# Kernel optimization log

Measured on AMD Instinct MI355X. Metric: run time of the kernel, lower is better.

The kernel has to match this reference:

```python
import jax, jax.numpy as jnp
import numpy as np

B, L, D = 1, 4096, 2048
H, KV, HD = 16, 4, 128
WINDOW = 1024
ROPE_BASE = 10000.0


def _rms_norm(x, scale):
    var = jnp.mean(jnp.square(x), axis=-1, keepdims=True)
    return x * jax.lax.rsqrt(var + 1e-6) * scale


def _apply_rope(x, positions, base_frequency):
    # x: (B, L, N, HD); positions: (B, L)
    head_dim = x.shape[-1]
    half = head_dim // 2
    freq_exp = 2.0 * jnp.arange(half, dtype=jnp.float32) / head_dim
    timescale = base_frequency ** freq_exp                       # (half,)
    sinusoid = positions[..., None].astype(jnp.float32) / timescale  # (B, L, half)
    sin = jnp.sin(sinusoid)[:, :, None, :]                       # (B, L, 1, half)
    cos = jnp.cos(sinusoid)[:, :, None, :]
    x1, x2 = x[..., :half], x[..., half:]
    return jnp.concatenate([x1 * cos - x2 * sin, x2 * cos + x1 * sin], axis=-1)


def setup_inputs() -> dict:
    key = jax.random.key(0)
    ks = jax.random.split(key, 5)
    x = jax.random.normal(ks[0], (B, L, D), dtype=jnp.float32)
    positions = jnp.broadcast_to(jnp.arange(L, dtype=jnp.int32), (B, L))
    s = D ** -0.5
    Wq = jax.random.normal(ks[1], (D, H * HD), dtype=jnp.float32) * s
    Wk = jax.random.normal(ks[2], (D, KV * HD), dtype=jnp.float32) * s
    Wv = jax.random.normal(ks[3], (D, KV * HD), dtype=jnp.float32) * s
    Wo = jax.random.normal(ks[4], (H * HD, D), dtype=jnp.float32) * ((H * HD) ** -0.5)
    q_scale = jnp.ones((HD,), dtype=jnp.float32)
    k_scale = jnp.ones((HD,), dtype=jnp.float32)
    return {"x": x, "positions": positions, "Wq": Wq, "Wk": Wk, "Wv": Wv,
            "Wo": Wo, "q_scale": q_scale, "k_scale": k_scale}


def reference(x, positions, Wq, Wk, Wv, Wo, q_scale, k_scale):
    q = (x @ Wq).reshape(B, L, H, HD)
    k = (x @ Wk).reshape(B, L, KV, HD)
    v = (x @ Wv).reshape(B, L, KV, HD)

    q = _apply_rope(_rms_norm(q, q_scale), positions, ROPE_BASE)
    k = _apply_rope(_rms_norm(k, k_scale), positions, ROPE_BASE)

    rep = H // KV
    k = jnp.repeat(k, rep, axis=2)   # (B, L, H, HD)
    v = jnp.repeat(v, rep, axis=2)

    scale = HD ** -0.5
    scores = jnp.einsum('bqhd,bkhd->bhqk', q, k) * scale  # (B, H, L, L)

    idx = jnp.arange(L)
    causal = idx[:, None] >= idx[None, :]
    window = idx[None, :] >= idx[:, None] - (WINDOW - 1)
    mask = causal & window
    scores = jnp.where(mask[None, None, :, :], scores, jnp.finfo(scores.dtype).min)
    attn = jax.nn.softmax(scores, axis=-1)

    out = jnp.einsum('bhqk,bkhd->bqhd', attn, v).reshape(B, L, H * HD)
    return out @ Wo
```

## Files before the change

kernel.cpp:

```cpp
#include <hip/hip_runtime.h>
#include <cstdint>
#include <cstddef>

typedef unsigned short u16;
typedef __attribute__((ext_vector_type(4))) float  float4v;
typedef __attribute__((ext_vector_type(4))) int    int4v;
typedef __attribute__((ext_vector_type(8))) short  short8v;
typedef __attribute__((ext_vector_type(4))) short  short4v;

#define L_SEQ 4096
#define NH 16
#define NKV 4
#define WND 1024

static __device__ __forceinline__ u16 f2bf(float f) {
  union { float f; unsigned u; } v; v.f = f;
  unsigned r = (v.u + 0x7FFFu + ((v.u >> 16) & 1u)) >> 16;
  return (u16)r;
}
static __device__ __forceinline__ float bf2f(u16 b) {
  union { unsigned u; float f; } v; v.u = ((unsigned)b) << 16;
  return v.f;
}

__global__ __launch_bounds__(256) void k_cvt(const float* __restrict__ in,
                                             u16* __restrict__ out, int n4) {
  int i = blockIdx.x * 256 + threadIdx.x;
  if (i >= n4) return;
  float4v v = ((const float4v*)in)[i];
  short4v o;
  o[0] = (short)f2bf(v[0]); o[1] = (short)f2bf(v[1]);
  o[2] = (short)f2bf(v[2]); o[3] = (short)f2bf(v[3]);
  ((short4v*)out)[i] = o;
}

__global__ __launch_bounds__(256) void k_transpose64(const float* __restrict__ in,
                                                     u16* __restrict__ out,
                                                     int K, int N, int row_off) {
  __shared__ float tile[64][65];
  int n0 = blockIdx.x * 64, k0 = blockIdx.y * 64;
  int tx = threadIdx.x & 63, ty = threadIdx.x >> 6;
#pragma unroll
  for (int i = 0; i < 16; i++)
    tile[ty + i*4][tx] = in[(size_t)(k0 + ty + i*4)*N + n0 + tx];
  __syncthreads();
#pragma unroll
  for (int i = 0; i < 16; i++)
    out[(size_t)(row_off + n0 + ty + i*4)*K + k0 + tx] = f2bf(tile[tx][ty + i*4]);
}

__global__ __launch_bounds__(256) void k_vtrans(const u16* __restrict__ qkvb,
                                                u16* __restrict__ vT) {
  __shared__ u16 tile[64][66];
  int p0 = blockIdx.x * 64, d0 = blockIdx.y * 64;
  int tx = threadIdx.x & 63, ty = threadIdx.x >> 6;
#pragma unroll
  for (int i = 0; i < 16; i++)
    tile[ty + i*4][tx] = qkvb[(size_t)(p0 + ty + i*4)*3072 + 2560 + d0 + tx];
  __syncthreads();
#pragma unroll
  for (int i = 0; i < 16; i++)
    vT[(size_t)(d0 + ty + i*4)*L_SEQ + p0 + tx] = tile[tx][ty + i*4];
}

template<int BF16_OUT>
__global__ __launch_bounds__(256) void k_gemm_bt(const u16* __restrict__ A,
                                                 const u16* __restrict__ B,
                                                 void* __restrict__ Cv,
                                                 int M, int N, int K) {
  __shared__ alignas(16) u16 As[128*64];
  __shared__ alignas(16) u16 Bs[128*64];
  int tid = threadIdx.x;
  int lane = tid & 63, wave = tid >> 6;
  int lr = lane & 15, lg = lane >> 4;
  int m0 = blockIdx.y * 128, n0 = blockIdx.x * 128;
  int wm = (wave >> 1) * 64, wn = (wave & 1) * 64;

  float4v acc[4][4];
#pragma unroll
  for (int i = 0; i < 4; i++)
#pragma unroll
    for (int j = 0; j < 4; j++)
#pragma unroll
      for (int r = 0; r < 4; r++) acc[i][j][r] = 0.f;

  for (int kt = 0; kt < K; kt += 64) {
    __syncthreads();
#pragma unroll
    for (int it = 0; it < 4; it++) {
      int s = it*256 + tid;
      int row = s >> 3, j = s & 7;
      int col = ((j ^ (row & 7)) << 3);
      __builtin_amdgcn_global_load_lds(
          (const __attribute__((address_space(1))) void*)(A + (size_t)(m0 + row)*K + kt + col),
          (__attribute__((address_space(3))) void*)(&As[s * 8]), 16, 0, 0);
      __builtin_amdgcn_global_load_lds(
          (const __attribute__((address_space(1))) void*)(B + (size_t)(n0 + row)*K + kt + col),
          (__attribute__((address_space(3))) void*)(&Bs[s * 8]), 16, 0, 0);
    }
    __syncthreads();
#pragma unroll
    for (int half = 0; half < 2; half++) {
      short8v af[4], bf[4];
#pragma unroll
      for (int i = 0; i < 4; i++) {
        int row = wm + i*16 + lr;
        af[i] = *(const short8v*)(&As[row*64 + ((((half<<2)|lg) ^ (row & 7)) << 3)]);
      }
#pragma unroll
      for (int j = 0; j < 4; j++) {
        int row = wn + j*16 + lr;
        bf[j] = *(const short8v*)(&Bs[row*64 + ((((half<<2)|lg) ^ (row & 7)) << 3)]);
      }
#pragma unroll
      for (int i = 0; i < 4; i++)
#pragma unroll
        for (int j = 0; j < 4; j++)
          acc[i][j] = __builtin_amdgcn_mfma_f32_16x16x32_bf16(af[i], bf[j], acc[i][j], 0, 0, 0);
    }
  }
#pragma unroll
  for (int i = 0; i < 4; i++)
#pragma unroll
    for (int j = 0; j < 4; j++)
#pragma unroll
      for (int r = 0; r < 4; r++) {
        size_t idx = (size_t)(m0 + wm + i*16 + lg*4 + r)*N + (n0 + wn + j*16 + lr);
        if (BF16_OUT) ((u16*)Cv)[idx] = f2bf(acc[i][j][r]);
        else          ((float*)Cv)[idx] = acc[i][j][r];
      }
}

__global__ __launch_bounds__(256) void k_qknorm(const u16* __restrict__ qkvb,
    const int* __restrict__ positions, const float* __restrict__ q_scale,
    const float* __restrict__ k_scale, u16* __restrict__ qb,
    u16* __restrict__ kb) {
  int p = blockIdx.x * 4 + (threadIdx.x >> 6);
  int l = threadIdx.x & 63;
  const float LOG2_BASE = 13.287712379549449f;
  float ang = (float)positions[p] * exp2f(-(float)l * (LOG2_BASE / 64.0f));
  float sn, cs; sincosf(ang, &sn, &cs);
  float qs1 = q_scale[l], qs2 = q_scale[l + 64];
  float ks1 = k_scale[l], ks2 = k_scale[l + 64];
  const u16* base = qkvb + (size_t)p * 3072;
  const float qsc = 0.08838834764831845f;
#pragma unroll
  for (int h = 0; h < 16; h++) {
    float x1 = bf2f(base[h*128 + l]), x2 = bf2f(base[h*128 + l + 64]);
    float ss = x1*x1 + x2*x2;
#pragma unroll
    for (int m = 1; m < 64; m <<= 1) ss += __shfl_xor(ss, m);
    float rinv = rsqrtf(ss * (1.0f/128.0f) + 1e-6f);
    x1 *= rinv * qs1; x2 *= rinv * qs2;
    u16* dst = qb + ((size_t)p*NH + h)*128;
    dst[l]      = f2bf((x1*cs - x2*sn) * qsc);
    dst[l + 64] = f2bf((x2*cs + x1*sn) * qsc);
  }
#pragma unroll
  for (int g = 0; g < 4; g++) {
    float x1 = bf2f(base[2048 + g*128 + l]), x2 = bf2f(base[2048 + g*128 + l + 64]);
    float ss = x1*x1 + x2*x2;
#pragma unroll
    for (int m = 1; m < 64; m <<= 1) ss += __shfl_xor(ss, m);
    float rinv = rsqrtf(ss * (1.0f/128.0f) + 1e-6f);
    x1 *= rinv * ks1; x2 *= rinv * ks2;
    u16* dst = kb + ((size_t)p*NKV + g)*128;
    dst[l]      = f2bf(x1*cs - x2*sn);
    dst[l + 64] = f2bf(x2*cs + x1*sn);
  }
}

__global__ __launch_bounds__(256) void k_attn(const u16* __restrict__ qb,
    const u16* __restrict__ kb, const u16* __restrict__ vT,
    u16* __restrict__ ob) {
  __shared__ alignas(16) u16 Ks[32*136];
  __shared__ alignas(16) u16 Vs[128*40];
  __shared__ alignas(16) u16 Pw[4][2][16*40];
  int tid = threadIdx.x;
  int lane = tid & 63, wave = tid >> 6;
  int lr = lane & 15, lg = lane >> 4;
  int gh = blockIdx.y;
  int h = gh * 4 + wave;
  int q0 = blockIdx.x * 32;
  const float LOG2E = 1.44269504088896f;

  short8v qf[2][4];
#pragma unroll
  for (int m = 0; m < 2; m++) {
    const u16* qrow = qb + ((size_t)(q0 + m*16 + lr)*NH + h)*128 + lg*8;
#pragma unroll
    for (int t = 0; t < 4; t++) qf[m][t] = *(const short8v*)(qrow + t*32);
  }

  float4v O[8][2];
#pragma unroll
  for (int dt = 0; dt < 8; dt++)
#pragma unroll
    for (int m = 0; m < 2; m++)
#pragma unroll
      for (int r = 0; r < 4; r++) O[dt][m][r] = 0.f;
  float lsum[2][4] = {{0.f,0.f,0.f,0.f},{0.f,0.f,0.f,0.f}};

  int kstart = q0 - (WND - 1); if (kstart < 0) kstart = 0; kstart &= ~31;
  for (int kt = kstart; kt < q0 + 32; kt += 32) {
    __syncthreads();
#pragma unroll
    for (int it = 0; it < 2; it++) {
      int c = it*256 + tid;
      { int row = c >> 4, cc = (c & 15) << 3;
        *(int4v*)(&Ks[row*136 + cc]) =
            *(const int4v*)(kb + ((size_t)(kt + row)*NKV + gh)*128 + cc); }
      { int row = c >> 2, cc = (c & 3) << 3;
        *(int4v*)(&Vs[row*40 + cc]) =
            *(const int4v*)(vT + (size_t)(gh*128 + row)*L_SEQ + kt + cc); }
    }
    __syncthreads();

    float4v S[2][2];
#pragma unroll
    for (int m = 0; m < 2; m++)
#pragma unroll
      for (int t2 = 0; t2 < 2; t2++)
#pragma unroll
        for (int r = 0; r < 4; r++) S[m][t2][r] = 0.f;
#pragma unroll
    for (int t2 = 0; t2 < 2; t2++)
#pragma unroll
      for (int t = 0; t < 4; t++) {
        short8v kf = *(const short8v*)(&Ks[(t2*16 + lr)*136 + t*32 + lg*8]);
        S[0][t2] = __builtin_amdgcn_mfma_f32_16x16x32_bf16(qf[0][t], kf, S[0][t2], 0, 0, 0);
        S[1][t2] = __builtin_amdgcn_mfma_f32_16x16x32_bf16(qf[1][t], kf, S[1][t2], 0, 0, 0);
      }

#pragma unroll
    for (int m = 0; m < 2; m++)
#pragma unroll
      for (int r = 0; r < 4; r++) {
        int pos = q0 + m*16 + lg*4 + r;
#pragma unroll
        for (int t2 = 0; t2 < 2; t2++) {
          int key = kt + t2*16 + lr;
          float p = (key > pos || key < pos - (WND - 1))
                      ? 0.f : exp2f(S[m][t2][r] * LOG2E);
          lsum[m][r] += p;
          Pw[wave][m][(lg*4 + r)*40 + t2*16 + lr] = f2bf(p);
        }
      }
    short8v pf[2];
#pragma unroll
    for (int m = 0; m < 2; m++)
      pf[m] = *(const short8v*)(&Pw[wave][m][lr*40 + lg*8]);

#pragma unroll
    for (int dt = 0; dt < 8; dt++) {
      short8v vf = *(const short8v*)(&Vs[(dt*16 + lr)*40 + lg*8]);
      O[dt][0] = __builtin_amdgcn_mfma_f32_16x16x32_bf16(pf[0], vf, O[dt][0], 0, 0, 0);
      O[dt][1] = __builtin_amdgcn_mfma_f32_16x16x32_bf16(pf[1], vf, O[dt][1], 0, 0, 0);
    }
  }

#pragma unroll
  for (int m = 0; m < 2; m++)
#pragma unroll
    for (int r = 0; r < 4; r++) {
      float s = lsum[m][r];
      s += __shfl_xor(s, 1); s += __shfl_xor(s, 2);
      s += __shfl_xor(s, 4); s += __shfl_xor(s, 8);
      float inv = 1.0f / s;
#pragma unroll
      for (int dt = 0; dt < 8; dt++)
        ob[((size_t)(q0 + m*16 + lg*4 + r)*NH + h)*128 + dt*16 + lr] =
            f2bf(O[dt][m][r] * inv);
    }
}

extern "C" void kernel_launch(void* const* d_in, const int* in_sizes, int n_in,
                              void* d_out, int out_size, void* d_ws, size_t ws_size,
                              hipStream_t stream) {
  (void)in_sizes; (void)n_in; (void)out_size; (void)ws_size;
  const float* x        = (const float*)d_in[0];
  const int*   positions= (const int*)d_in[1];
  const float* Wq       = (const float*)d_in[2];
  const float* Wk       = (const float*)d_in[3];
  const float* Wv       = (const float*)d_in[4];
  const float* Wo       = (const float*)d_in[5];
  const float* q_scale  = (const float*)d_in[6];
  const float* k_scale  = (const float*)d_in[7];
  float* out = (float*)d_out;

  char* ws = (char*)d_ws;
  u16* xb   = (u16*)ws; ws += (size_t)4096*2048*2;
  u16* Wt   = (u16*)ws; ws += (size_t)3072*2048*2;
  u16* Wot  = (u16*)ws; ws += (size_t)2048*2048*2;
  u16* qkvb = (u16*)ws; ws += (size_t)4096*3072*2;
  u16* qb   = (u16*)ws; ws += (size_t)4096*2048*2;
  u16* kb   = (u16*)ws; ws += (size_t)4096*512*2;
  u16* vT   = (u16*)ws; ws += (size_t)4096*512*2;
  u16* ob   = qkvb;

  k_cvt<<<8192, 256, 0, stream>>>(x, xb, 2097152);
  k_transpose64<<<dim3(32,32), 256, 0, stream>>>(Wq, Wt, 2048, 2048, 0);
  k_transpose64<<<dim3(8,32),  256, 0, stream>>>(Wk, Wt, 2048, 512, 2048);
  k_transpose64<<<dim3(8,32),  256, 0, stream>>>(Wv, Wt, 2048, 512, 2560);
  k_transpose64<<<dim3(32,32), 256, 0, stream>>>(Wo, Wot, 2048, 2048, 0);
  k_gemm_bt<1><<<dim3(24,32), 256, 0, stream>>>(xb, Wt, qkvb, 4096, 3072, 2048);
  k_qknorm<<<1024, 256, 0, stream>>>(qkvb, positions, q_scale, k_scale, qb, kb);
  k_vtrans<<<dim3(64,8), 256, 0, stream>>>(qkvb, vT);
  k_attn<<<dim3(128,4), 256, 0, stream>>>(qb, kb, vT, ob);
  k_gemm_bt<0><<<dim3(16,32), 256, 0, stream>>>(ob, Wot, out, 4096, 2048, 2048);
}
```

Baseline: 316.2 us.

## Restructure attention kernel: 64-key tiles, direct LDS loads, swizzle, MFMA row sums

The attention kernel now processes 64 keys per iteration and loads K/V tiles with global_load_lds directly into XOR-swizzled shared memory instead of padded register-staged copies. The log2(e) factor is folded into the Q scale, so the kernel takes exp2 directly. Masking is skipped for tiles fully inside the window. Softmax row sums come from an extra MFMA against a ones vector instead of per-lane sums and shuffles. Blocks are remapped so each XCD handles one KV group, and bf16 rounding uses a cheaper round-half-up, which slightly changes numerics.

```diff
diff --git a/kernel.cpp b/kernel.cpp
--- a/kernel.cpp
+++ b/kernel.cpp
@@ -17,6 +17,10 @@
   union { float f; unsigned u; } v; v.f = f;
   unsigned r = (v.u + 0x7FFFu + ((v.u >> 16) & 1u)) >> 16;
   return (u16)r;
+}
+static __device__ __forceinline__ u16 f2bf_fast(float f) {
+  union { float f; unsigned u; } v; v.f = f;
+  return (u16)((v.u + 0x8000u) >> 16);
 }
 static __device__ __forceinline__ float bf2f(u16 b) {
   union { unsigned u; float f; } v; v.u = ((unsigned)b) << 16;
@@ -143,7 +147,7 @@
   float qs1 = q_scale[l], qs2 = q_scale[l + 64];
   float ks1 = k_scale[l], ks2 = k_scale[l + 64];
   const u16* base = qkvb + (size_t)p * 3072;
-  const float qsc = 0.08838834764831845f;
+  const float qsc = 0.12751741505539613f;
 #pragma unroll
   for (int h = 0; h < 16; h++) {
     float x1 = bf2f(base[h*128 + l]), x2 = bf2f(base[h*128 + l + 64]);
@@ -173,16 +177,17 @@
 __global__ __launch_bounds__(256) void k_attn(const u16* __restrict__ qb,
     const u16* __restrict__ kb, const u16* __restrict__ vT,
     u16* __restrict__ ob) {
-  __shared__ alignas(16) u16 Ks[32*136];
-  __shared__ alignas(16) u16 Vs[128*40];
-  __shared__ alignas(16) u16 Pw[4][2][16*40];
+  __shared__ alignas(16) u16 Ks[64*128];
+  __shared__ alignas(16) u16 Vs[128*64];
+  __shared__ alignas(16) u16 Pw[4][2][16*72];
   int tid = threadIdx.x;
   int lane = tid & 63, wave = tid >> 6;
   int lr = lane & 15, lg = lane >> 4;
-  int gh = blockIdx.y;
+  int flat = blockIdx.x;
+  int xcd = flat & 7, slot = flat >> 3;
+  int gh = xcd >> 1;
+  int q0 = ((xcd & 1) * 64 + slot) * 32;
   int h = gh * 4 + wave;
-  int q0 = blockIdx.x * 32;
-  const float LOG2E = 1.44269504088896f;
 
   short8v qf[2][4];
 #pragma unroll
@@ -192,70 +197,96 @@
     for (int t = 0; t < 4; t++) qf[m][t] = *(const short8v*)(qrow + t*32);
   }
 
-  float4v O[8][2];
-#pragma unroll
-  for (int dt = 0; dt < 8; dt++)
+  const short one_bf = (short)0x3F80;
+  const short8v ones = {one_bf,one_bf,one_bf,one_bf,one_bf,one_bf,one_bf,one_bf};
+
+  float4v O[9][2];
+#pragma unroll
+  for (int dt = 0; dt < 9; dt++)
 #pragma unroll
     for (int m = 0; m < 2; m++)
 #pragma unroll
       for (int r = 0; r < 4; r++) O[dt][m][r] = 0.f;
-  float lsum[2][4] = {{0.f,0.f,0.f,0.f},{0.f,0.f,0.f,0.f}};
-
-  int kstart = q0 - (WND - 1); if (kstart < 0) kstart = 0; kstart &= ~31;
-  for (int kt = kstart; kt < q0 + 32; kt += 32) {
+
+  int kstart = q0 - (WND - 1); if (kstart < 0) kstart = 0; kstart &= ~63;
+  for (int kt = kstart; kt < q0 + 32; kt += 64) {
     __syncthreads();
 #pragma unroll
-    for (int it = 0; it < 2; it++) {
-      int c = it*256 + tid;
-      { int row = c >> 4, cc = (c & 15) << 3;
-        *(int4v*)(&Ks[row*136 + cc]) =
-            *(const int4v*)(kb + ((size_t)(kt + row)*NKV + gh)*128 + cc); }
-      { int row = c >> 2, cc = (c & 3) << 3;
-        *(int4v*)(&Vs[row*40 + cc]) =
-            *(const int4v*)(vT + (size_t)(gh*128 + row)*L_SEQ + kt + cc); }
+    for (int it = 0; it < 4; it++) {
+      int s = it*256 + tid;
+      { int row = s >> 4, j = s & 15, col = (j ^ (row & 15)) << 3;
+        __builtin_amdgcn_global_load_lds(
+            (const __attribute__((address_space(1))) void*)(kb + (size_t)(kt + row)*512 + gh*128 + col),
+            (__attribute__((address_space(3))) void*)(&Ks[s * 8]), 16, 0, 0); }
+      { int row = s >> 3, j = s & 7, col = (j ^ (row & 7)) << 3;
+        __builtin_amdgcn_global_load_lds(
+            (const __attribute__((address_space(1))) void*)(vT + (size_t)(gh*128 + row)*L_SEQ + kt + col),
+            (__attribute__((address_space(3))) void*)(&Vs[s * 8]), 16, 0, 0); }
     }
     __syncthreads();
 
-    float4v S[2][2];
+    float4v S[2][4];
 #pragma unroll
     for (int m = 0; m < 2; m++)
 #pragma unroll
-      for (int t2 = 0; t2 < 2; t2++)
+      for (int t2 = 0; t2 < 4; t2++)
 #pragma unroll
         for (int r = 0; r < 4; r++) S[m][t2][r] = 0.f;
 #pragma unroll
-    for (int t2 = 0; t2 < 2; t2++)
+    for (int t2 = 0; t2 < 4; t2++) {
+      int row = t2*16 + lr;
 #pragma unroll
       for (int t = 0; t < 4; t++) {
-        short8v kf = *(const short8v*)(&Ks[(t2*16 + lr)*136 + t*32 + lg*8]);
+        short8v kf = *(const short8v*)(&Ks[row*128 + (((t*4 + lg) ^ (row & 15)) << 3)]);
         S[0][t2] = __builtin_amdgcn_mfma_f32_16x16x32_bf16(qf[0][t], kf, S[0][t2], 0, 0, 0);
         S[1][t2] = __builtin_amdgcn_mfma_f32_16x16x32_bf16(qf[1][t], kf, S[1][t2], 0, 0, 0);
       }
-
+    }
+
+    bool need_mask = (kt + 64 > q0) || (kt < q0 - (WND - 32));
+    if (need_mask) {
+#pragma unroll
+      for (int m = 0; m < 2; m++)
+#pragma unroll
+        for (int r = 0; r < 4; r++) {
+          int pos = q0 + m*16 + lg*4 + r;
+#pragma unroll
+          for (int t2 = 0; t2 < 4; t2++) {
+            int key = kt + t2*16 + lr;
+            float p = (key > pos || key < pos - (WND - 1)) ? 0.f : exp2f(S[m][t2][r]);
+            Pw[wave][m][(lg*4 + r)*72 + t2*16 + lr] = f2bf_fast(p);
+          }
+        }
+    } else {
+#pragma unroll
+      for (int m = 0; m < 2; m++)
+#pragma unroll
+        for (int r = 0; r < 4; r++)
+#pragma unroll
+          for (int t2 = 0; t2 < 4; t2++)
+            Pw[wave][m][(lg*4 + r)*72 + t2*16 + lr] = f2bf_fast(exp2f(S[m][t2][r]));
+    }
+
+    short8v pf[2][2];
 #pragma unroll
     for (int m = 0; m < 2; m++)
 #pragma unroll
-      for (int r = 0; r < 4; r++) {
-        int pos = q0 + m*16 + lg*4 + r;
-#pragma unroll
-        for (int t2 = 0; t2 < 2; t2++) {
-          int key = kt + t2*16 + lr;
-          float p = (key > pos || key < pos - (WND - 1))
-                      ? 0.f : exp2f(S[m][t2][r] * LOG2E);
-          lsum[m][r] += p;
-          Pw[wave][m][(lg*4 + r)*40 + t2*16 + lr] = f2bf(p);
-        }
-      }
-    short8v pf[2];
-#pragma unroll
-    for (int m = 0; m < 2; m++)
-      pf[m] = *(const short8v*)(&Pw[wave][m][lr*40 + lg*8]);
-
-#pragma unroll
-    for (int dt = 0; dt < 8; dt++) {
-      short8v vf = *(const short8v*)(&Vs[(dt*16 + lr)*40 + lg*8]);
-      O[dt][0] = __builtin_amdgcn_mfma_f32_16x16x32_bf16(pf[0], vf, O[dt][0], 0, 0, 0);
-      O[dt][1] = __builtin_amdgcn_mfma_f32_16x16x32_bf16(pf[1], vf, O[dt][1], 0, 0, 0);
+      for (int sub = 0; sub < 2; sub++)
+        pf[m][sub] = *(const short8v*)(&Pw[wave][m][lr*72 + sub*32 + lg*8]);
+
+#pragma unroll
+    for (int sub = 0; sub < 2; sub++)
+#pragma unroll
+      for (int dt = 0; dt < 8; dt++) {
+        int row = dt*16 + lr;
+        short8v vf = *(const short8v*)(&Vs[row*64 + (((sub*4 + lg) ^ (row & 7)) << 3)]);
+        O[dt][0] = __builtin_amdgcn_mfma_f32_16x16x32_bf16(pf[0][sub], vf, O[dt][0], 0, 0, 0);
+        O[dt][1] = __builtin_amdgcn_mfma_f32_16x16x32_bf16(pf[1][sub], vf, O[dt][1], 0, 0, 0);
+      }
+#pragma unroll
+    for (int m = 0; m < 2; m++) {
+      O[8][m] = __builtin_amdgcn_mfma_f32_16x16x32_bf16(pf[m][0], ones, O[8][m], 0, 0, 0);
+      O[8][m] = __builtin_amdgcn_mfma_f32_16x16x32_bf16(pf[m][1], ones, O[8][m], 0, 0, 0);
     }
   }
 
@@ -263,10 +294,7 @@
   for (int m = 0; m < 2; m++)
 #pragma unroll
     for (int r = 0; r < 4; r++) {
-      float s = lsum[m][r];
-      s += __shfl_xor(s, 1); s += __shfl_xor(s, 2);
-      s += __shfl_xor(s, 4); s += __shfl_xor(s, 8);
-      float inv = 1.0f / s;
+      float inv = 1.0f / O[8][m][r];
 #pragma unroll
       for (int dt = 0; dt < 8; dt++)
         ob[((size_t)(q0 + m*16 + lg*4 + r)*NH + h)*128 + dt*16 + lr] =
@@ -306,6 +334,6 @@
   k_gemm_bt<1><<<dim3(24,32), 256, 0, stream>>>(xb, Wt, qkvb, 4096, 3072, 2048);
   k_qknorm<<<1024, 256, 0, stream>>>(qkvb, positions, q_scale, k_scale, qb, kb);
   k_vtrans<<<dim3(64,8), 256, 0, stream>>>(qkvb, vT);
-  k_attn<<<dim3(128,4), 256, 0, stream>>>(qb, kb, vT, ob);
+  k_attn<<<512, 256, 0, stream>>>(qb, kb, vT, ob);
   k_gemm_bt<0><<<dim3(16,32), 256, 0, stream>>>(ob, Wot, out, 4096, 2048, 2048);
 }
```

Measured after the change: 288.9 us. 1.09x faster.
